# Performance work log

Hardware: AMD Instinct MI355X
Metric: run time of the kernel (lower is better)

## Reference

```python
import jax, jax.numpy as jnp
import numpy as np

EMBED_DIM = 1024
NUM_HEADS = 16
HEAD_DIM = EMBED_DIM // NUM_HEADS
B, S = 4, 2048


def setup_inputs() -> dict:
    key = jax.random.key(0)
    ks = jax.random.split(key, 11)
    d = EMBED_DIM
    s = 1.0 / np.sqrt(d)
    return {
        "query": jax.random.normal(ks[0], (B, S, d), jnp.float32),
        "key": jax.random.normal(ks[1], (B, S, d), jnp.float32),
        "value": jax.random.normal(ks[2], (B, S, d), jnp.float32),
        "Wq": jax.random.normal(ks[3], (d, d), jnp.float32) * s,
        "bq": jnp.zeros((d,), jnp.float32),
        "Wk": jax.random.normal(ks[4], (d, d), jnp.float32) * s,
        "bk": jnp.zeros((d,), jnp.float32),
        "Wv": jax.random.normal(ks[5], (d, d), jnp.float32) * s,
        "bv": jnp.zeros((d,), jnp.float32),
        "Wo": jax.random.normal(ks[6], (d, d), jnp.float32) * s,
        "bo": jnp.zeros((d,), jnp.float32),
    }


def reference(query, key, value, Wq, bq, Wk, bk, Wv, bv, Wo, bo):
    b, t, d = query.shape
    s = key.shape[1]
    h, hd = NUM_HEADS, HEAD_DIM
    # Linear projections (torch Linear: x @ W.T + b)
    q = (query @ Wq.T + bq).reshape(b, t, h, hd).transpose(0, 2, 1, 3)  # [B,H,T,hd]
    k = (key @ Wk.T + bk).reshape(b, s, h, hd).transpose(0, 2, 1, 3)    # [B,H,S,hd]
    v = (value @ Wv.T + bv).reshape(b, s, h, hd).transpose(0, 2, 1, 3)  # [B,H,S,hd]
    scale = 1.0 / np.sqrt(hd).astype(np.float32)
    attn = jnp.einsum('bhtd,bhsd->bhts', q, k) * scale  # [B,H,T,S]
    attn = jax.nn.softmax(attn, axis=-1)
    out = jnp.einsum('bhts,bhsd->bhtd', attn, v)        # [B,H,T,hd]
    out = out.transpose(0, 2, 1, 3).reshape(b, t, d)    # [B,T,D]
    out = out @ Wo.T + bo
    return out
```

## Files before the change

### kernel.cpp

```cpp
#include <hip/hip_runtime.h>
#include <hip/hip_bf16.h>
#include <stdint.h>

typedef __attribute__((ext_vector_type(8))) short short8;
typedef __attribute__((ext_vector_type(4))) float floatx4;
typedef __attribute__((ext_vector_type(16))) float floatx16;
typedef __attribute__((ext_vector_type(4))) uint16_t ushort4v;

#define MFMA16(a, b, c) __builtin_amdgcn_mfma_f32_16x16x32_bf16((a), (b), (c), 0, 0, 0)
#define MFMA32(a, b, c) __builtin_amdgcn_mfma_f32_32x32x16_bf16((a), (b), (c), 0, 0, 0)

#define GLOAD_LDS16(g, l)                                                          \
  __builtin_amdgcn_global_load_lds(                                                \
      (const __attribute__((address_space(1))) uint32_t*)(g),                      \
      (__attribute__((address_space(3))) uint32_t*)(l), 16, 0, 0)

#define CVTPK(lo_, hi_, out_) \
  asm("v_cvt_pk_bf16_f32 %0, %1, %2" : "=v"(out_) : "v"(lo_), "v"(hi_))
#define SWAP32(a_, b_) \
  asm("v_permlane32_swap_b32 %0, %1" : "+v"(a_), "+v"(b_))

__device__ __forceinline__ uint16_t f2bf(float x) {
  union { float f; uint32_t u; } c; c.f = x;
  return (uint16_t)((c.u + 0x7FFFu + ((c.u >> 16) & 1u)) >> 16);
}

__global__ void cvt3_k(const float* __restrict__ s0, const float* __restrict__ s1,
                       const float* __restrict__ s2, uint16_t* __restrict__ dst, int n4) {
  const float* src = blockIdx.z == 0 ? s0 : (blockIdx.z == 1 ? s1 : s2);
  uint16_t* d = dst + (size_t)blockIdx.z * 8388608;
  int stride = gridDim.x * blockDim.x;
  for (int i = blockIdx.x * blockDim.x + threadIdx.x; i < n4; i += stride) {
    float4 v = ((const float4*)src)[i];
    ushort4v o;
    o.x = f2bf(v.x); o.y = f2bf(v.y); o.z = f2bf(v.z); o.w = f2bf(v.w);
    ((ushort4v*)d)[i] = o;
  }
}
__global__ void cvt4_k(const float* __restrict__ s0, const float* __restrict__ s1,
                       const float* __restrict__ s2, const float* __restrict__ s3,
                       uint16_t* __restrict__ dst, int n4) {
  const float* src = blockIdx.z == 0 ? s0 : (blockIdx.z == 1 ? s1 : (blockIdx.z == 2 ? s2 : s3));
  uint16_t* d = dst + (size_t)blockIdx.z * 1048576;
  int stride = gridDim.x * blockDim.x;
  for (int i = blockIdx.x * blockDim.x + threadIdx.x; i < n4; i += stride) {
    float4 v = ((const float4*)src)[i];
    ushort4v o;
    o.x = f2bf(v.x); o.y = f2bf(v.y); o.z = f2bf(v.z); o.w = f2bf(v.w);
    ((ushort4v*)d)[i] = o;
  }
}

template <int OUT_BF16>
__device__ __forceinline__ void gemm_body(const uint16_t* __restrict__ A,
                                          const uint16_t* __restrict__ W,
                                          const float* __restrict__ bias,
                                          void* __restrict__ Cout, float scale,
                                          int brow, int bcol) {
  constexpr int N = 1024, K = 1024;
  __shared__ uint16_t As[128 * 32];
  __shared__ uint16_t Bs[128 * 32];
  const int t = threadIdx.x;
  const int l = t & 63;
  const int w = t >> 6;
  const int wr = w >> 1, wc = w & 1;
  const int l16 = l & 15, lhi = l >> 4;

  floatx4 acc[4][4] = {};

  for (int k0 = 0; k0 < K; k0 += 32) {
#pragma unroll
    for (int j = 0; j < 2; ++j) {
      int c = j * 256 + t;
      int row = c >> 2;
      int ko = (c & 3) * 8;
      const uint16_t* ga = A + (size_t)(brow + row) * K + k0 + ko;
      const uint16_t* gb = W + (size_t)(bcol + row) * K + k0 + ko;
      uint16_t* la = As + (size_t)(j * 256 + w * 64) * 8;
      uint16_t* lb = Bs + (size_t)(j * 256 + w * 64) * 8;
      GLOAD_LDS16(ga, la);
      GLOAD_LDS16(gb, lb);
    }
    __syncthreads();

    short8 a[4], b[4];
#pragma unroll
    for (int m = 0; m < 4; ++m)
      a[m] = *(const short8*)&As[(wr * 64 + m * 16 + l16) * 32 + lhi * 8];
#pragma unroll
    for (int n = 0; n < 4; ++n)
      b[n] = *(const short8*)&Bs[(wc * 64 + n * 16 + l16) * 32 + lhi * 8];
#pragma unroll
    for (int m = 0; m < 4; ++m)
#pragma unroll
      for (int n = 0; n < 4; ++n)
        acc[m][n] = MFMA16(a[m], b[n], acc[m][n]);
    __syncthreads();
  }

#pragma unroll
  for (int n = 0; n < 4; ++n) {
    int col = bcol + wc * 64 + n * 16 + l16;
    float bv = bias[col];
#pragma unroll
    for (int m = 0; m < 4; ++m) {
#pragma unroll
      for (int j = 0; j < 4; ++j) {
        int row = brow + wr * 64 + m * 16 + lhi * 4 + j;
        float v = (acc[m][n][j] + bv) * scale;
        if (OUT_BF16)
          ((uint16_t*)Cout)[(size_t)row * N + col] = f2bf(v);
        else
          ((float*)Cout)[(size_t)row * N + col] = v;
      }
    }
  }
}

__global__ __launch_bounds__(256)
void gemm_qkv_k(const uint16_t* __restrict__ XQ, const uint16_t* __restrict__ XK,
                const uint16_t* __restrict__ XV, const uint16_t* __restrict__ WQ,
                const uint16_t* __restrict__ WK, const uint16_t* __restrict__ WV,
                const float* __restrict__ bq, const float* __restrict__ bk,
                const float* __restrict__ bv, uint16_t* __restrict__ QP,
                uint16_t* __restrict__ KP, uint16_t* __restrict__ VP, float qscale) {
  const int f = (blockIdx.z * 64 + blockIdx.y) * 8 + blockIdx.x;
  const int virt = (f & 7) * 192 + (f >> 3);
  const int vz = virt >> 9;
  const int vy = (virt & 511) >> 3;
  const int vx = virt & 7;

  const uint16_t *A, *W; const float* bi; uint16_t* C; float sc;
  if (vz == 0)      { A = XQ; W = WQ; bi = bq; C = QP; sc = qscale; }
  else if (vz == 1) { A = XK; W = WK; bi = bk; C = KP; sc = 1.0f; }
  else              { A = XV; W = WV; bi = bv; C = VP; sc = 1.0f; }
  gemm_body<1>(A, W, bi, C, sc, vy * 128, vx * 128);
}

__global__ __launch_bounds__(256)
void gemm_o_k(const uint16_t* __restrict__ A, const uint16_t* __restrict__ W,
              const float* __restrict__ bias, float* __restrict__ Cout) {
  const int f = blockIdx.y * 8 + blockIdx.x;
  const int virt = (f & 7) * 64 + (f >> 3);
  const int vy = virt >> 3;
  const int vx = virt & 7;
  gemm_body<0>(A, W, bias, Cout, 1.0f, vy * 128, vx * 128);
}

__global__ __launch_bounds__(256)
void vtrans_k(const uint16_t* __restrict__ VP, uint16_t* __restrict__ VT) {
  __shared__ uint16_t T[64][66];
  const int t = threadIdx.x;
  const int bh = blockIdx.y;
  const int s0 = blockIdx.x * 64;
  const int b = bh >> 4, h = bh & 15;
  const size_t src = ((size_t)b * 2048 + s0) * 1024 + (size_t)h * 64;
#pragma unroll
  for (int it = 0; it < 2; ++it) {
    int u = it * 256 + t;
    int s = u >> 3;
    int d0 = (u & 7) * 8;
    short8 v = *(const short8*)(VP + src + (size_t)s * 1024 + d0);
#pragma unroll
    for (int i = 0; i < 8; ++i) T[s][d0 + i] = (uint16_t)v[i];
  }
  __syncthreads();
  const size_t dst = (size_t)bh * 131072 + s0;
#pragma unroll
  for (int it = 0; it < 2; ++it) {
    int u = it * 256 + t;
    int d = u >> 3;
    int ss = (u & 7) * 8;
    union { uint16_t u16[8]; short8 s8; } pk;
#pragma unroll
    for (int i = 0; i < 8; ++i) pk.u16[i] = T[ss + i][d];
    *(short8*)(VT + dst + (size_t)d * 2048 + ss) = pk.s8;
  }
}

__global__ __launch_bounds__(512, 2)
void attn_k(const uint16_t* __restrict__ Qp, const uint16_t* __restrict__ Kp,
            const uint16_t* __restrict__ Vt, uint16_t* __restrict__ AO) {
  __shared__ uint16_t Kl[2][64 * 128];
  __shared__ uint16_t Vl[2][64 * 128];

  const int t = threadIdx.x;
  const int l = t & 63, w = t >> 6;
  const int l32 = l & 31, hi = l >> 5;

  const int f = blockIdx.y * 8 + blockIdx.x;
  const int virt = (f & 7) * 64 + (f >> 3);
  const int vx = virt & 7;
  const int vy = virt >> 3;

  const int q0 = vx * 256 + w * 32;
  const size_t base = (size_t)(vy >> 4) * 2048 * 1024 + (size_t)(vy & 15) * 64;
  const size_t vbg = (size_t)vy * 131072;

  union PAu { uint32_t u[4]; short8 s; };

  const uint16_t* pK[2];
  const uint16_t* pV[2];
#pragma unroll
  for (int i = 0; i < 2; ++i) {
    int c = i * 512 + t;
    int r = c >> 4, qs = c & 15;
    int q0c = qs ^ (r & 15);
    pK[i] = Kp + base + (size_t)(64 * (q0c >> 3) + r) * 1024 + (q0c & 7) * 8;
    pV[i] = Vt + vbg + (size_t)r * 2048 + q0c * 8;
  }

#define STAGE_ALL(NB)                                                 \
  {                                                                   \
    _Pragma("unroll") for (int i = 0; i < 2; ++i) {                   \
      GLOAD_LDS16(pK[i], &Kl[NB][(size_t)(i * 512 + w * 64) * 8]);    \
      GLOAD_LDS16(pV[i], &Vl[NB][(size_t)(i * 512 + w * 64) * 8]);    \
      pK[i] += 131072;                          \
      pV[i] += 128;                             \
    }                                                                 \
  }

  short8 qf[4];
#pragma unroll
  for (int ks = 0; ks < 4; ++ks)
    qf[ks] = *(const short8*)(Qp + base + (size_t)(q0 + l32) * 1024 + ks * 16 + hi * 8);

  floatx16 of0 = {}, of1 = {};
  float rs = 0.f;

  const int swzb = (l32 & 15);
  const int krow = l32 * 256;

  STAGE_ALL(0);
  __syncthreads();

#define QK_Q(SF, CUR, H, RH)                                                          \
  {                                                                                   \
    _Pragma("unroll") for (int ks = 0; ks < 4; ++ks) {                                \
      int kbyte = krow + (RH) * 8192 + ((((H) * 8 + 2 * ks + hi) ^ swzb) << 4);       \
      short8 kf = *(const short8*)((char*)Kl[CUR] + kbyte);                           \
      SF = MFMA32(kf, qf[ks], SF);                                                    \
    }                                                                                 \
  }

#define EXPPACK(SF, P0, P1)                                                           \
  {                                                                                   \
    _Pragma("unroll") for (int r = 0; r < 16; ++r) {                                  \
      SF[r] = __builtin_amdgcn_exp2f(SF[r]);                                          \
      rs += SF[r];                                                                    \
    }                                                                                 \
    uint32_t a0, a1, b0, b1;                                                          \
    CVTPK(SF[0], SF[1], a0); CVTPK(SF[2], SF[3], a1);                                 \
    CVTPK(SF[4], SF[5], b0); CVTPK(SF[6], SF[7], b1);                                 \
    SWAP32(a0, b0); SWAP32(a1, b1);                                                   \
    P0.u[0] = a0; P0.u[1] = a1; P0.u[2] = b0; P0.u[3] = b1;                           \
    CVTPK(SF[8], SF[9], a0); CVTPK(SF[10], SF[11], a1);                               \
    CVTPK(SF[12], SF[13], b0); CVTPK(SF[14], SF[15], b1);                             \
    SWAP32(a0, b0); SWAP32(a1, b1);                                                   \
    P1.u[0] = a0; P1.u[1] = a1; P1.u[2] = b0; P1.u[3] = b1;                           \
  }

#define PV_Q(P0, P1, CUR, H, RH)                                                      \
  {                                                                                   \
    int vb0 = krow + ((((H) * 8 + 2 * (2 * (RH)) + hi) ^ swzb) << 4);                 \
    int vb1 = krow + ((((H) * 8 + 2 * (2 * (RH) + 1) + hi) ^ swzb) << 4);             \
    short8 vf00 = *(const short8*)((char*)Vl[CUR] + vb0);                             \
    short8 vf01 = *(const short8*)((char*)Vl[CUR] + vb0 + 8192);                      \
    short8 vf10 = *(const short8*)((char*)Vl[CUR] + vb1);                             \
    short8 vf11 = *(const short8*)((char*)Vl[CUR] + vb1 + 8192);                      \
    of0 = MFMA32(P0.s, vf00, of0);                                                    \
    of1 = MFMA32(P0.s, vf01, of1);                                                    \
    of0 = MFMA32(P1.s, vf10, of0);                                                    \
    of1 = MFMA32(P1.s, vf11, of1);                                                    \
  }

#define STEP128(CUR, PF)                                                              \
  {                                                                                   \
    if (PF) STAGE_ALL(CUR ^ 1);                                                       \
    floatx16 sfA = {}, sfB = {};                                                      \
    QK_Q(sfA, CUR, 0, 0);                                                             \
    QK_Q(sfB, CUR, 0, 1);                                                             \
    {                                                                                 \
      PAu p0, p1;                                                                     \
      EXPPACK(sfA, p0, p1);                                                           \
      PV_Q(p0, p1, CUR, 0, 0);                                                        \
    }                                                                                 \
    sfA = (floatx16){};                                                               \
    QK_Q(sfA, CUR, 1, 0);                                                             \
    {                                                                                 \
      PAu p0, p1;                                                                     \
      EXPPACK(sfB, p0, p1);                                                           \
      PV_Q(p0, p1, CUR, 0, 1);                                                        \
    }                                                                                 \
    sfB = (floatx16){};                                                               \
    QK_Q(sfB, CUR, 1, 1);                                                             \
    {                                                                                 \
      PAu p0, p1;                                                                     \
      EXPPACK(sfA, p0, p1);                                                           \
      PV_Q(p0, p1, CUR, 1, 0);                                                        \
    }                                                                                 \
    {                                                                                 \
      PAu p0, p1;                                                                     \
      EXPPACK(sfB, p0, p1);                                                           \
      PV_Q(p0, p1, CUR, 1, 1);                                                        \
    }                                                                                 \
    __syncthreads();                                                                  \
  }

  for (int it = 0; it < 8; ++it) {
    STEP128(0, 1);
    STEP128(1, it < 7);
  }

  rs += __shfl_xor(rs, 32);
#pragma unroll
  for (int r = 0; r < 16; ++r) {
    int qloc = (r & 3) + 8 * (r >> 2) + 4 * hi;
    float rsq = __shfl(rs, qloc);
    float rinv = 1.0f / rsq;
    int qrow = q0 + qloc;
    AO[base + (size_t)qrow * 1024 + l32]      = f2bf(of0[r] * rinv);
    AO[base + (size_t)qrow * 1024 + 32 + l32] = f2bf(of1[r] * rinv);
  }
#undef STAGE_ALL
#undef QK_Q
#undef EXPPACK
#undef PV_Q
#undef STEP128
}

extern "C" void kernel_launch(void* const* d_in, const int* in_sizes, int n_in,
                              void* d_out, int out_size, void* d_ws, size_t ws_size,
                              hipStream_t stream) {
  const float* q  = (const float*)d_in[0];
  const float* k  = (const float*)d_in[1];
  const float* v  = (const float*)d_in[2];
  const float* Wq = (const float*)d_in[3];
  const float* bq = (const float*)d_in[4];
  const float* Wk = (const float*)d_in[5];
  const float* bk = (const float*)d_in[6];
  const float* Wv = (const float*)d_in[7];
  const float* bv = (const float*)d_in[8];
  const float* Wo = (const float*)d_in[9];
  const float* bo = (const float*)d_in[10];

  const size_t MB = 1ull << 20;
  char* ws = (char*)d_ws;
  uint16_t* XQ  = (uint16_t*)(ws + 0 * MB);
  uint16_t* XK  = (uint16_t*)(ws + 16 * MB);
  uint16_t* XV  = (uint16_t*)(ws + 32 * MB);
  uint16_t* WQb = (uint16_t*)(ws + 48 * MB);
  uint16_t* WKb = (uint16_t*)(ws + 50 * MB);
  uint16_t* WVb = (uint16_t*)(ws + 52 * MB);
  uint16_t* WOb = (uint16_t*)(ws + 54 * MB);
  uint16_t* QP  = (uint16_t*)(ws + 56 * MB);
  uint16_t* KP  = (uint16_t*)(ws + 72 * MB);
  uint16_t* VP  = (uint16_t*)(ws + 88 * MB);
  uint16_t* AO  = XQ;
  uint16_t* VT  = XK;

  const int NTOK = 4 * 2048;
  const int D = 1024;
  const int nBig = NTOK * D / 4;
  const int nW = D * D / 4;
  const float qscale = 0.125f * 1.4426950408889634f;

  cvt3_k<<<dim3(2048, 1, 3), dim3(256), 0, stream>>>(q, k, v, XQ, nBig);
  cvt4_k<<<dim3(1024, 1, 4), dim3(256), 0, stream>>>(Wq, Wk, Wv, Wo, WQb, nW);

  gemm_qkv_k<<<dim3(D / 128, NTOK / 128, 3), dim3(256), 0, stream>>>(
      XQ, XK, XV, WQb, WKb, WVb, bq, bk, bv, QP, KP, VP, qscale);

  vtrans_k<<<dim3(32, 64), dim3(256), 0, stream>>>(VP, VT);

  attn_k<<<dim3(8, 64), dim3(512), 0, stream>>>(QP, KP, VT, AO);

  gemm_o_k<<<dim3(D / 128, NTOK / 128), dim3(256), 0, stream>>>(AO, WOb, bo, (float*)d_out);
}
```

Baseline: 203.3 us.

## Fuse V transpose into QKV GEMM epilogue and swizzle GEMM LDS layout

The V projection epilogue now writes its bf16 output directly in the per-head transposed [B*H, d, S] layout the attention kernel reads, which removes the separate vtrans kernel launch and its round trip through global memory. The GEMM shared-memory tiles are also rearranged into a 32x128 layout with an XOR swizzle on the 16-byte chunks, aimed at reducing LDS bank conflicts on the MFMA operand reads. The cost is that the transposed V stores are strided 8-byte writes in the GEMM epilogue rather than contiguous row writes.

```diff
diff --git a/kernel.cpp b/kernel.cpp
--- a/kernel.cpp
+++ b/kernel.cpp
@@ -51,15 +51,15 @@
   }
 }
 
-template <int OUT_BF16>
+template <int MODE>
 __device__ __forceinline__ void gemm_body(const uint16_t* __restrict__ A,
                                           const uint16_t* __restrict__ W,
                                           const float* __restrict__ bias,
                                           void* __restrict__ Cout, float scale,
                                           int brow, int bcol) {
   constexpr int N = 1024, K = 1024;
-  __shared__ uint16_t As[128 * 32];
-  __shared__ uint16_t Bs[128 * 32];
+  __shared__ uint16_t As[32 * 128];
+  __shared__ uint16_t Bs[32 * 128];
   const int t = threadIdx.x;
   const int l = t & 63;
   const int w = t >> 6;
@@ -72,24 +72,28 @@
 #pragma unroll
     for (int j = 0; j < 2; ++j) {
       int c = j * 256 + t;
-      int row = c >> 2;
-      int ko = (c & 3) * 8;
-      const uint16_t* ga = A + (size_t)(brow + row) * K + k0 + ko;
-      const uint16_t* gb = W + (size_t)(bcol + row) * K + k0 + ko;
-      uint16_t* la = As + (size_t)(j * 256 + w * 64) * 8;
-      uint16_t* lb = Bs + (size_t)(j * 256 + w * 64) * 8;
-      GLOAD_LDS16(ga, la);
-      GLOAD_LDS16(gb, lb);
+      int r = c >> 4, qs = c & 15;
+      int q0 = qs ^ (r & 15);
+      int arow = 32 * (q0 >> 2) + r;
+      int ko = (q0 & 3) * 8;
+      const uint16_t* ga = A + (size_t)(brow + arow) * K + k0 + ko;
+      const uint16_t* gb = W + (size_t)(bcol + arow) * K + k0 + ko;
+      GLOAD_LDS16(ga, As + (size_t)(j * 256 + w * 64) * 8);
+      GLOAD_LDS16(gb, Bs + (size_t)(j * 256 + w * 64) * 8);
     }
     __syncthreads();
 
     short8 a[4], b[4];
 #pragma unroll
-    for (int m = 0; m < 4; ++m)
-      a[m] = *(const short8*)&As[(wr * 64 + m * 16 + l16) * 32 + lhi * 8];
-#pragma unroll
-    for (int n = 0; n < 4; ++n)
-      b[n] = *(const short8*)&Bs[(wc * 64 + n * 16 + l16) * 32 + lhi * 8];
+    for (int m = 0; m < 4; ++m) {
+      int ar = wr * 64 + m * 16 + l16;
+      a[m] = *(const short8*)&As[(ar & 31) * 128 + ((((ar >> 5) * 4 + lhi) ^ (ar & 15))) * 8];
+    }
+#pragma unroll
+    for (int n = 0; n < 4; ++n) {
+      int br_ = wc * 64 + n * 16 + l16;
+      b[n] = *(const short8*)&Bs[(br_ & 31) * 128 + ((((br_ >> 5) * 4 + lhi) ^ (br_ & 15))) * 8];
+    }
 #pragma unroll
     for (int m = 0; m < 4; ++m)
 #pragma unroll
@@ -102,16 +106,29 @@
   for (int n = 0; n < 4; ++n) {
     int col = bcol + wc * 64 + n * 16 + l16;
     float bv = bias[col];
-#pragma unroll
-    for (int m = 0; m < 4; ++m) {
-#pragma unroll
-      for (int j = 0; j < 4; ++j) {
-        int row = brow + wr * 64 + m * 16 + lhi * 4 + j;
-        float v = (acc[m][n][j] + bv) * scale;
-        if (OUT_BF16)
-          ((uint16_t*)Cout)[(size_t)row * N + col] = f2bf(v);
-        else
-          ((float*)Cout)[(size_t)row * N + col] = v;
+    if (MODE == 2) {
+      int h = col >> 6, d = col & 63;
+#pragma unroll
+      for (int m = 0; m < 4; ++m) {
+        int row = brow + wr * 64 + m * 16 + lhi * 4;
+        int b_ = row >> 11, s = row & 2047;
+        union { uint16_t u[4]; ushort4v v; } pk4;
+#pragma unroll
+        for (int j = 0; j < 4; ++j) pk4.u[j] = f2bf(acc[m][n][j] + bv);
+        *(ushort4v*)((uint16_t*)Cout + (size_t)(b_ * 16 + h) * 131072 + (size_t)d * 2048 + s) = pk4.v;
+      }
+    } else {
+#pragma unroll
+      for (int m = 0; m < 4; ++m) {
+#pragma unroll
+        for (int j = 0; j < 4; ++j) {
+          int row = brow + wr * 64 + m * 16 + lhi * 4 + j;
+          float v = (acc[m][n][j] + bv) * scale;
+          if (MODE == 1)
+            ((uint16_t*)Cout)[(size_t)row * N + col] = f2bf(v);
+          else
+            ((float*)Cout)[(size_t)row * N + col] = v;
+        }
       }
     }
   }
@@ -123,18 +140,16 @@
                 const uint16_t* __restrict__ WK, const uint16_t* __restrict__ WV,
                 const float* __restrict__ bq, const float* __restrict__ bk,
                 const float* __restrict__ bv, uint16_t* __restrict__ QP,
-                uint16_t* __restrict__ KP, uint16_t* __restrict__ VP, float qscale) {
+                uint16_t* __restrict__ KP, uint16_t* __restrict__ VT, float qscale) {
   const int f = (blockIdx.z * 64 + blockIdx.y) * 8 + blockIdx.x;
   const int virt = (f & 7) * 192 + (f >> 3);
   const int vz = virt >> 9;
   const int vy = (virt & 511) >> 3;
   const int vx = virt & 7;
 
-  const uint16_t *A, *W; const float* bi; uint16_t* C; float sc;
-  if (vz == 0)      { A = XQ; W = WQ; bi = bq; C = QP; sc = qscale; }
-  else if (vz == 1) { A = XK; W = WK; bi = bk; C = KP; sc = 1.0f; }
-  else              { A = XV; W = WV; bi = bv; C = VP; sc = 1.0f; }
-  gemm_body<1>(A, W, bi, C, sc, vy * 128, vx * 128);
+  if (vz == 0)      gemm_body<1>(XQ, WQ, bq, QP, qscale, vy * 128, vx * 128);
+  else if (vz == 1) gemm_body<1>(XK, WK, bk, KP, 1.0f,  vy * 128, vx * 128);
+  else              gemm_body<2>(XV, WV, bv, VT, 1.0f,  vy * 128, vx * 128);
 }
 
 __global__ __launch_bounds__(256)
@@ -145,37 +160,6 @@
   const int vy = virt >> 3;
   const int vx = virt & 7;
   gemm_body<0>(A, W, bias, Cout, 1.0f, vy * 128, vx * 128);
-}
-
-__global__ __launch_bounds__(256)
-void vtrans_k(const uint16_t* __restrict__ VP, uint16_t* __restrict__ VT) {
-  __shared__ uint16_t T[64][66];
-  const int t = threadIdx.x;
-  const int bh = blockIdx.y;
-  const int s0 = blockIdx.x * 64;
-  const int b = bh >> 4, h = bh & 15;
-  const size_t src = ((size_t)b * 2048 + s0) * 1024 + (size_t)h * 64;
-#pragma unroll
-  for (int it = 0; it < 2; ++it) {
-    int u = it * 256 + t;
-    int s = u >> 3;
-    int d0 = (u & 7) * 8;
-    short8 v = *(const short8*)(VP + src + (size_t)s * 1024 + d0);
-#pragma unroll
-    for (int i = 0; i < 8; ++i) T[s][d0 + i] = (uint16_t)v[i];
-  }
-  __syncthreads();
-  const size_t dst = (size_t)bh * 131072 + s0;
-#pragma unroll
-  for (int it = 0; it < 2; ++it) {
-    int u = it * 256 + t;
-    int d = u >> 3;
-    int ss = (u & 7) * 8;
-    union { uint16_t u16[8]; short8 s8; } pk;
-#pragma unroll
-    for (int i = 0; i < 8; ++i) pk.u16[i] = T[ss + i][d];
-    *(short8*)(VT + dst + (size_t)d * 2048 + ss) = pk.s8;
-  }
 }
 
 __global__ __launch_bounds__(512, 2)
@@ -355,9 +339,8 @@
   uint16_t* WOb = (uint16_t*)(ws + 54 * MB);
   uint16_t* QP  = (uint16_t*)(ws + 56 * MB);
   uint16_t* KP  = (uint16_t*)(ws + 72 * MB);
-  uint16_t* VP  = (uint16_t*)(ws + 88 * MB);
+  uint16_t* VT  = (uint16_t*)(ws + 88 * MB);
   uint16_t* AO  = XQ;
-  uint16_t* VT  = XK;
 
   const int NTOK = 4 * 2048;
   const int D = 1024;
@@ -369,9 +352,7 @@
   cvt4_k<<<dim3(1024, 1, 4), dim3(256), 0, stream>>>(Wq, Wk, Wv, Wo, WQb, nW);
 
   gemm_qkv_k<<<dim3(D / 128, NTOK / 128, 3), dim3(256), 0, stream>>>(
-      XQ, XK, XV, WQb, WKb, WVb, bq, bk, bv, QP, KP, VP, qscale);
-
-  vtrans_k<<<dim3(32, 64), dim3(256), 0, stream>>>(VP, VT);
+      XQ, XK, XV, WQb, WKb, WVb, bq, bk, bv, QP, KP, VT, qscale);
 
   attn_k<<<dim3(8, 64), dim3(512), 0, stream>>>(QP, KP, VT, AO);
 
```

New measurement: 196.5 us, median of 2. 3.4% less time.
